# Kernel optimization log

Measured on AMD Instinct MI355X. Metric: run time of the kernel, lower is better.

The kernel has to match this reference:

```python
import jax, jax.numpy as jnp
import numpy as np

NUM_TARGETS = 2
N_ITER = 20
REF_MIC = 1          # 1-based reference mic
CONTRAST = 'laplace'
GAMMA = 1.0
PROJ_BACK = 'mdp'
TOL = 1e-5
EPS_R = 1e-10
REG = 1e-6


def contrast_weights(r, func, gamma, eps_r):
    # phi(r) = g'(r) / r for the chosen contrast function
    r = jnp.maximum(r, eps_r)
    if func == 'laplace':
        return 1.0 / (2.0 * r)
    if func == 'gaussian':
        return jnp.ones_like(r)
    if func == 'power':
        return gamma * r ** (gamma - 2.0)
    raise ValueError(func)


def _iva_forward(X):
    M, T, F, _ = X.shape
    K = NUM_TARGETS
    # (M,T,F,2) real/imag -> complex (F,M,T)
    X_c = jnp.transpose(X[..., 0] + 1j * X[..., 1], (2, 0, 1))
    cdtype = X_c.dtype
    eyeM = jnp.eye(M, dtype=cdtype)
    W_hat = jnp.tile(eyeM[None], (F, 1, 1))
    W_hat = W_hat.at[:, K:, K:].set(-jnp.eye(M - K, dtype=cdtype))
    # input covariance (constant over iterations): (F,M,M)
    C = jnp.einsum('fmt,fnt->fmn', X_c, X_c.conj()) / T
    reg_eye = REG * eyeM  # broadcasts over F / (K,F)
    eps = jnp.finfo(jnp.float32).eps
    done = jnp.array(False)

    for _ in range(N_ITER):
        W_old = W_hat
        # current target estimates: (F,K,T)
        Y = jnp.einsum('fkm,fmt->fkt', W_hat[:, :K, :], X_c)
        r = jnp.sqrt(jnp.maximum((jnp.abs(Y) ** 2).sum(axis=0), EPS_R))  # (K,T)
        w_t = contrast_weights(r, CONTRAST, GAMMA, EPS_R).astype(cdtype)
        # weighted covariances: (K,F,M,M)
        V = jnp.einsum('kt,fmt,fnt->kfmn', w_t, X_c, X_c.conj()) / T
        V_reg = V + reg_eye

        Wn = W_hat
        for k in range(K):
            temp = Wn @ V_reg[k]                              # (F,M,M)
            e_k = jnp.zeros((F, M), dtype=cdtype).at[:, k].set(1.0)
            w_vec = jnp.linalg.solve(temp, e_k[..., None])[..., 0]  # (F,M)
            denom = jnp.sqrt(
                jnp.einsum('fm,fmn,fn->f', w_vec.conj(), V_reg[k], w_vec).real + EPS_R
            )
            Wn = Wn.at[:, k, :].set((w_vec / denom[:, None]).conj())
        # background block: J = solve(tmp[:, :, :K], tmp[:, :, K:])^H
        tmp = Wn[:, :K, :] @ C                                # (F,K,M)
        J = jnp.conj(jnp.swapaxes(jnp.linalg.solve(tmp[:, :, :K], tmp[:, :, K:]), 1, 2))
        Wn = Wn.at[:, K:, :K].set(J)

        rel = jnp.linalg.norm(Wn - W_old) / jnp.maximum(jnp.linalg.norm(W_old), eps)
        W_hat = jnp.where(done, W_old, Wn)  # freeze once converged (mimics break)
        done = done | (rel < TOL)

    W = W_hat[:, :K, :]
    Y = jnp.einsum('fkm,fmt->fkt', W, X_c)  # (F,K,T)
    if REF_MIC is not None and 0 < REF_MIC <= M:
        if PROJ_BACK == 'mdp':
            A = jnp.linalg.pinv(W)               # (F,M,K)
            scale = A[:, REF_MIC - 1, :]         # (F,K)
            Y = scale[:, :, None] * Y
        elif PROJ_BACK == 'scale_constraint':
            Wp = jnp.linalg.pinv(W)
            d = jnp.max(jnp.abs(Wp), axis=1)     # (F,K)
            Y = d[:, :, None].astype(cdtype) * Y
    Y_out = jnp.transpose(Y, (1, 2, 0))          # (K,T,F)
    return jnp.stack([Y_out.real, Y_out.imag], axis=-1)


def setup_inputs() -> dict:
    key = jax.random.key(0)
    X = jax.random.normal(key, (8, 2048, 513, 2), dtype=jnp.float32)
    return {"X": X}


def reference(X):
    return _iva_forward(X)
```

## Files before the change

kernel.cpp:

```cpp
#include <hip/hip_runtime.h>

#define F_ 513
#define M_ 8
#define T_ 2048
#define K_ 2
#define NITER 20
#define REGC 1e-6
#define EPSR 1e-10
#define TOLC 1e-5
#define NG 256
#define TS 4
#define UPB ((F_ + 3) / 4)

typedef double2 cd;
__device__ __forceinline__ cd cmk(double r, double i){ cd z; z.x=r; z.y=i; return z; }
__device__ __forceinline__ cd cadd(cd a, cd b){ return cmk(a.x+b.x, a.y+b.y); }
__device__ __forceinline__ cd csub(cd a, cd b){ return cmk(a.x-b.x, a.y-b.y); }
__device__ __forceinline__ cd cmul(cd a, cd b){ return cmk(a.x*b.x - a.y*b.y, a.x*b.y + a.y*b.x); }
__device__ __forceinline__ cd cconj(cd a){ return cmk(a.x, -a.y); }
__device__ __forceinline__ cd cdiv(cd a, cd b){
  double d = b.x*b.x + b.y*b.y;
  return cmk((a.x*b.x + a.y*b.y)/d, (a.y*b.x - a.x*b.y)/d);
}
__device__ __forceinline__ double cabs2(cd a){ return a.x*a.x + a.y*a.y; }
__device__ __forceinline__ cd shflc(cd v, int l){
  cd r; r.x = __shfl(v.x, l, 64); r.y = __shfl(v.y, l, 64); return r;
}
__device__ __forceinline__ cd sel8(const cd x[8], int idx){
  cd r = x[0];
  #pragma unroll
  for (int q=1;q<8;++q) if (idx==q) r = x[q];
  return r;
}

__device__ __forceinline__ void solve_f(int f, int lane,
    const cd* __restrict__ Vp, const cd* __restrict__ Cp,
    float2* __restrict__ Wg, double* __restrict__ dsum, double* __restrict__ osum)
{
  int i = lane >> 3, j = lane & 7;
  float2 wf = Wg[(size_t)f*64 + lane];
  cd Wn = cmk(wf.x, wf.y);
  cd Wold = Wn;
  cd x[8];
  #pragma unroll
  for (int k=0; k<K_; ++k){
    cd Vr = cmk(0,0);
    #pragma unroll
    for (int s2=0; s2<TS; ++s2)
      Vr = cadd(Vr, Vp[(((size_t)k*F_ + f)*TS + s2)*64 + lane]);
    if (i == j) Vr.x += REGC;
    cd temp = cmk(0,0);
    #pragma unroll
    for (int q=0;q<8;++q) temp = cadd(temp, cmul(shflc(Wn, i*8+q), shflc(Vr, q*8+j)));
    cd b = cmk(i==k ? 1.0 : 0.0, 0.0);
    for (int p=0; p<8; ++p){
      double pv = (j==p && i>=p) ? cabs2(temp) : -1.0;
      int pidx = i;
      for (int off=32; off; off>>=1){
        double ov = __shfl_xor(pv, off, 64);
        int oi = __shfl_xor(pidx, off, 64);
        if (ov > pv){ pv = ov; pidx = oi; }
      }
      cd tp = shflc(temp, pidx*8 + j);
      cd tq = shflc(temp, p*8 + j);
      cd bp_ = shflc(b, pidx*8 + j);
      cd bq_ = shflc(b, p*8 + j);
      if (i == p){ temp = tp; b = bp_; }
      else if (i == pidx){ temp = tq; b = bq_; }
      cd tip = shflc(temp, i*8 + p);
      cd tpp = shflc(temp, p*8 + p);
      cd tpj = shflc(temp, p*8 + j);
      cd bpr = shflc(b, p*8 + j);
      cd fac = cdiv(tip, tpp);
      if (i > p){ temp = csub(temp, cmul(fac, tpj)); b = csub(b, cmul(fac, bpr)); }
    }
    #pragma unroll
    for (int p=7; p>=0; --p){
      cd s = shflc(b, p*8);
      #pragma unroll
      for (int q=p+1; q<8; ++q){
        cd tpq = shflc(temp, p*8 + q);
        s = csub(s, cmul(tpq, x[q]));
      }
      x[p] = cdiv(s, shflc(temp, p*8 + p));
    }
    cd xi = sel8(x, i), xj = sel8(x, j);
    cd z = cmul(cconj(xi), Vr);
    double dl = z.x*xj.x - z.y*xj.y;
    for (int off=32; off; off>>=1) dl += __shfl_xor(dl, off, 64);
    double denom = sqrt(dl + EPSR);
    if (i == k){ Wn = cmk(xj.x/denom, -xj.y/denom); }
  }
  cd Cc = cmk(0,0);
  #pragma unroll
  for (int s2=0; s2<TS; ++s2)
    Cc = cadd(Cc, Cp[((size_t)f*TS + s2)*64 + lane]);
  cd tmp = cmk(0,0);
  #pragma unroll
  for (int q=0;q<8;++q) tmp = cadd(tmp, cmul(shflc(Wn, i*8+q), shflc(Cc, q*8+j)));
  cd A = shflc(tmp, 0), B = shflc(tmp, 1), C2 = shflc(tmp, 8), D = shflc(tmp, 9);
  cd det = csub(cmul(A,D), cmul(B,C2));
  cd t0 = shflc(tmp, i);
  cd t1 = shflc(tmp, 8 + i);
  cd Z0 = cdiv(csub(cmul(D,t0), cmul(B,t1)), det);
  cd Z1 = cdiv(csub(cmul(A,t1), cmul(C2,t0)), det);
  if (i >= K_ && j < K_){
    cd Z = (j==0) ? Z0 : Z1;
    Wn = cconj(Z);
  }
  double ds = cabs2(csub(Wn, Wold));
  double os = cabs2(Wold);
  for (int off=32; off; off>>=1){
    ds += __shfl_xor(ds, off, 64);
    os += __shfl_xor(os, off, 64);
  }
  float2 wo; wo.x = (float)Wn.x; wo.y = (float)Wn.y;
  Wg[(size_t)f*64 + lane] = wo;
  if (lane == 0){ dsum[f] = ds; osum[f] = os; }
}

__global__ __launch_bounds__(256) void pack_kernel(const float2* __restrict__ Xin, float2* __restrict__ Xc){
  __shared__ float tr[32][65];
  __shared__ float ti[32][65];
  int f0 = blockIdx.x*64, t0 = blockIdx.y*32, m = blockIdx.z;
  for (int i = threadIdx.x; i < 32*64; i += 256){
    int tl = i >> 6, fl = i & 63;
    int f = f0 + fl;
    float2 v; v.x = 0.f; v.y = 0.f;
    if (f < F_) v = Xin[((size_t)m*T_ + (t0 + tl))*F_ + f];
    tr[tl][fl] = v.x; ti[tl][fl] = v.y;
  }
  __syncthreads();
  for (int i = threadIdx.x; i < 64*16; i += 256){
    int fl = i >> 4, tl2 = i & 15;
    int f = f0 + fl;
    if (f < F_){
      int t = 2*tl2;
      float4 v;
      v.x = tr[t][fl];   v.y = ti[t][fl];
      v.z = tr[t+1][fl]; v.w = ti[t+1][fl];
      *(float4*)&Xc[((size_t)f*8 + m)*T_ + t0 + t] = v;
    }
  }
}

__global__ __launch_bounds__(512) void cov0_kernel(const float2* __restrict__ Xc, cd* __restrict__ Cp,
                                                   float2* __restrict__ Wg){
  __shared__ float2 xs[8][514];
  __shared__ double wred[2][8][64];
  int f = blockIdx.x, s = blockIdx.y;
  int tid = threadIdx.x;
  int w = tid >> 6, lane = tid & 63;
  int m = lane >> 3, n = lane & 7;
  if (s == 0 && tid < 64){
    int i = tid >> 3, j = tid & 7;
    float v = (i==j) ? (i < K_ ? 1.f : -1.f) : 0.f;
    Wg[(size_t)f*64 + tid] = make_float2(v, 0.f);
  }
  #pragma unroll
  for (int r=0; r<4; ++r){
    int idx = tid + r*512;
    int mm = idx >> 8, q = idx & 255;
    float4 v = ((const float4*)(Xc + ((size_t)f*8 + mm)*T_ + s*512))[q];
    *(float4*)&xs[mm][q*2] = v;
  }
  __syncthreads();
  const float2* xm = xs[m];
  const float2* xn = xs[n];
  int tbase = w*64;
  float ar=0.f, ai=0.f;
  #pragma unroll 8
  for (int tt=0; tt<64; tt+=2){
    float4 av = *(const float4*)&xm[tbase+tt];
    float4 bv = *(const float4*)&xn[tbase+tt];
    ar += fmaf(av.x, bv.x, av.y*bv.y) + fmaf(av.z, bv.z, av.w*bv.w);
    ai += fmaf(av.y, bv.x, -av.x*bv.y) + fmaf(av.w, bv.z, -av.z*bv.w);
  }
  wred[0][w][lane] = ar; wred[1][w][lane] = ai;
  __syncthreads();
  if (tid < 64){
    double sr=0, si=0;
    #pragma unroll
    for (int ww=0; ww<8; ++ww){ sr += wred[0][ww][tid]; si += wred[1][ww][tid]; }
    const double inv = 1.0/(double)T_;
    Cp[((size_t)f*TS + s)*64 + tid] = cmk(sr*inv, si*inv);
  }
}

__global__ __launch_bounds__(256) void yr_kernel(const float2* __restrict__ Xc, const float2* __restrict__ Wg,
                                                 float* __restrict__ part, const int* __restrict__ flags){
  if (*(volatile const int*)flags) return;
  int g = blockIdx.y;
  int t = blockIdx.x*256 + threadIdx.x;
  float acc0 = 0.f, acc1 = 0.f;
  for (int f = g; f < F_; f += NG){
    const float2* Wf = Wg + (size_t)f*64;
    float2 y0; y0.x=0; y0.y=0;
    float2 y1; y1.x=0; y1.y=0;
    #pragma unroll
    for (int m=0;m<8;++m){
      float2 xv = Xc[((size_t)f*8 + m)*T_ + t];
      float2 w0 = Wf[m];
      float2 w1 = Wf[8+m];
      y0.x = fmaf(w0.x,xv.x,fmaf(-w0.y,xv.y,y0.x)); y0.y = fmaf(w0.x,xv.y,fmaf(w0.y,xv.x,y0.y));
      y1.x = fmaf(w1.x,xv.x,fmaf(-w1.y,xv.y,y1.x)); y1.y = fmaf(w1.x,xv.y,fmaf(w1.y,xv.x,y1.y));
    }
    acc0 += y0.x*y0.x + y0.y*y0.y;
    acc1 += y1.x*y1.x + y1.y*y1.y;
  }
  part[((size_t)g*2+0)*T_ + t] = acc0;
  part[((size_t)g*2+1)*T_ + t] = acc1;
}

__global__ __launch_bounds__(256) void rw_kernel(const float* __restrict__ part, float* __restrict__ wts2f,
                                                 const int* __restrict__ flags){
  if (*(volatile const int*)flags) return;
  int v = blockIdx.x*256 + threadIdx.x;
  int k = v >> 11, t = v & (T_-1);
  double s = 0;
  for (int g=0; g<NG; ++g) s += (double)part[((size_t)g*2+k)*T_ + t];
  wts2f[2*t + k] = (float)(0.5 / sqrt(fmax(s, EPSR)));
}

__global__ __launch_bounds__(512, 8) void covF_kernel(const float2* __restrict__ Xc, const float2* __restrict__ wts2,
                                                      cd* __restrict__ Vp, const int* __restrict__ flags){
  if (*(volatile const int*)flags) return;
  __shared__ float2 xs[8][514];
  __shared__ float2 wsm2[512];
  int f = blockIdx.x, s = blockIdx.y;
  int tid = threadIdx.x;
  int w = tid >> 6, lane = tid & 63;
  int m = lane >> 3, n = lane & 7;
  #pragma unroll
  for (int r=0; r<4; ++r){
    int idx = tid + r*512;
    int mm = idx >> 8, q = idx & 255;
    float4 v = ((const float4*)(Xc + ((size_t)f*8 + mm)*T_ + s*512))[q];
    *(float4*)&xs[mm][q*2] = v;
  }
  wsm2[tid] = wts2[s*512 + tid];
  __syncthreads();
  const float2* xm = xs[m];
  const float2* xn = xs[n];
  int tbase = w*64;
  float a0r=0.f, a0i=0.f, a1r=0.f, a1i=0.f;
  #pragma unroll 8
  for (int tt=0; tt<64; tt+=2){
    float4 av = *(const float4*)&xm[tbase+tt];
    float4 bv = *(const float4*)&xn[tbase+tt];
    float zr0 = fmaf(av.x, bv.x, av.y*bv.y);
    float zi0 = fmaf(av.y, bv.x, -av.x*bv.y);
    float zr1 = fmaf(av.z, bv.z, av.w*bv.w);
    float zi1 = fmaf(av.w, bv.z, -av.z*bv.w);
    float4 wv = *(const float4*)&wsm2[tbase+tt];
    a0r = fmaf(wv.x, zr0, a0r); a0i = fmaf(wv.x, zi0, a0i);
    a1r = fmaf(wv.y, zr0, a1r); a1i = fmaf(wv.y, zi0, a1i);
    a0r = fmaf(wv.z, zr1, a0r); a0i = fmaf(wv.z, zi1, a0i);
    a1r = fmaf(wv.w, zr1, a1r); a1i = fmaf(wv.w, zi1, a1i);
  }
  __syncthreads();
  float* wred = (float*)&xs[0][0];
  wred[0*512 + w*64 + lane] = a0r;
  wred[1*512 + w*64 + lane] = a0i;
  wred[2*512 + w*64 + lane] = a1r;
  wred[3*512 + w*64 + lane] = a1i;
  __syncthreads();
  const double inv = 1.0/(double)T_;
  if (tid < 128){
    int k = tid >> 6, l = tid & 63;
    float rr = 0.f, ii = 0.f;
    #pragma unroll
    for (int ww=0; ww<8; ++ww){
      rr += wred[(k*2+0)*512 + ww*64 + l];
      ii += wred[(k*2+1)*512 + ww*64 + l];
    }
    Vp[(((size_t)k*F_ + f)*TS + s)*64 + l] = cmk((double)rr*inv, (double)ii*inv);
  }
}

__global__ __launch_bounds__(256) void updF_kernel(const cd* __restrict__ Vp, const cd* __restrict__ Cp,
                                                   float2* __restrict__ Wg,
                                                   double* __restrict__ dsum, double* __restrict__ osum,
                                                   int* __restrict__ flags){
  if (*(volatile const int*)flags) return;
  int lane = threadIdx.x & 63;
  int w = threadIdx.x >> 6;
  int f = blockIdx.x*4 + w;
  if (f < F_) solve_f(f, lane, Vp, Cp, Wg, dsum, osum);
  __shared__ int lastFlag;
  __threadfence();
  __syncthreads();
  if (threadIdx.x == 0){
    int tk = atomicAdd(&flags[1], 1);
    lastFlag = (tk == UPB-1) ? 1 : 0;
  }
  __syncthreads();
  if (lastFlag && threadIdx.x < 64){
    __threadfence();
    double d=0, o=0;
    for (int idx=lane; idx<F_; idx+=64){
      d += ((volatile double*)dsum)[idx];
      o += ((volatile double*)osum)[idx];
    }
    for (int off=32; off; off>>=1){ d += __shfl_xor(d, off, 64); o += __shfl_xor(o, off, 64); }
    if (lane == 0){
      flags[1] = 0;
      double rel = sqrt(d) / fmax(sqrt(o), 1.1920928955078125e-7);
      if (rel < TOLC) flags[0] = 1;
    }
  }
}

__global__ __launch_bounds__(256) void out_kernel(const float2* __restrict__ Xc, const float2* __restrict__ Wg,
                                                  float2* __restrict__ out){
  __shared__ float re0[32][65], im0[32][65], re1[32][65], im1[32][65];
  __shared__ float2 scl[32][2];
  int f0 = blockIdx.x*32, t0 = blockIdx.y*64;
  int lane = threadIdx.x & 63, w = threadIdx.x >> 6;
  if (threadIdx.x < 32){
    int f = f0 + threadIdx.x;
    if (f < F_){
      cd w0[8], w1[8];
      #pragma unroll
      for (int m=0;m<8;++m){
        float2 a = Wg[(size_t)f*64 + m];     w0[m] = cmk(a.x, a.y);
        float2 b = Wg[(size_t)f*64 + 8 + m]; w1[m] = cmk(b.x, b.y);
      }
      cd G00 = cmk(0,0), G01 = cmk(0,0), G11 = cmk(0,0);
      #pragma unroll
      for (int m=0;m<8;++m){
        G00 = cadd(G00, cmul(w0[m], cconj(w0[m])));
        G01 = cadd(G01, cmul(w0[m], cconj(w1[m])));
        G11 = cadd(G11, cmul(w1[m], cconj(w1[m])));
      }
      cd G10 = cconj(G01);
      cd det = csub(cmul(G00,G11), cmul(G01,G10));
      cd I00 = cdiv(G11, det), I01 = cdiv(cmk(-G01.x,-G01.y), det);
      cd I10 = cdiv(cmk(-G10.x,-G10.y), det), I11 = cdiv(G00, det);
      cd c0 = cconj(w0[0]), c1 = cconj(w1[0]);
      cd s0 = cadd(cmul(c0, I00), cmul(c1, I10));
      cd s1 = cadd(cmul(c0, I01), cmul(c1, I11));
      scl[threadIdx.x][0] = make_float2((float)s0.x, (float)s0.y);
      scl[threadIdx.x][1] = make_float2((float)s1.x, (float)s1.y);
    }
  }
  __syncthreads();
  for (int fl = w; fl < 32; fl += 4){
    int f = f0 + fl;
    if (f < F_){
      const float2* Wf = Wg + (size_t)f*64;
      int t = t0 + lane;
      float2 y0; y0.x=0; y0.y=0;
      float2 y1; y1.x=0; y1.y=0;
      #pragma unroll
      for (int m=0;m<8;++m){
        float2 xv = Xc[((size_t)f*8 + m)*T_ + t];
        float2 w0 = Wf[m];
        float2 w1 = Wf[8+m];
        y0.x += w0.x*xv.x - w0.y*xv.y; y0.y += w0.x*xv.y + w0.y*xv.x;
        y1.x += w1.x*xv.x - w1.y*xv.y; y1.y += w1.x*xv.y + w1.y*xv.x;
      }
      float2 s0 = scl[fl][0];
      float2 s1 = scl[fl][1];
      re0[fl][lane] = s0.x*y0.x - s0.y*y0.y; im0[fl][lane] = s0.x*y0.y + s0.y*y0.x;
      re1[fl][lane] = s1.x*y1.x - s1.y*y1.y; im1[fl][lane] = s1.x*y1.y + s1.y*y1.x;
    }
  }
  __syncthreads();
  for (int i = threadIdx.x; i < 32*64; i += 256){
    int tl = i >> 5, fl = i & 31;
    int f = f0 + fl;
    if (f < F_){
      int t = t0 + tl;
      float2 o0; o0.x = re0[fl][tl]; o0.y = im0[fl][tl];
      float2 o1; o1.x = re1[fl][tl]; o1.y = im1[fl][tl];
      out[((size_t)(0*T_ + t))*F_ + f] = o0;
      out[((size_t)(1*T_ + t))*F_ + f] = o1;
    }
  }
}

extern "C" void kernel_launch(void* const* d_in, const int* in_sizes, int n_in,
                              void* d_out, int out_size, void* d_ws, size_t ws_size,
                              hipStream_t stream) {
  const float2* Xin = (const float2*)d_in[0];
  char* ws = (char*)d_ws;
  size_t off = 0;
  auto alloc = [&](size_t bytes) -> void* {
    void* p = ws + off;
    off += (bytes + 255) & ~(size_t)255;
    return p;
  };
  float2* Xc   = (float2*)alloc((size_t)F_*M_*T_*8);
  cd*     Cp   = (cd*)alloc((size_t)F_*TS*64*16);
  cd*     Vp   = (cd*)alloc((size_t)K_*F_*TS*64*16);
  float2* W    = (float2*)alloc((size_t)F_*64*8);
  float*  part = (float*)alloc((size_t)NG*K_*T_*4);
  float*  wts2 = (float*)alloc((size_t)T_*8);
  double* dsum = (double*)alloc((size_t)F_*8);
  double* osum = (double*)alloc((size_t)F_*8);
  int*    ibuf = (int*)alloc(4096);
  if (off > ws_size) return;
  int* flags = ibuf;

  hipMemsetAsync(ibuf, 0, 4096, stream);

  pack_kernel<<<dim3(9, 64, 8), 256, 0, stream>>>(Xin, Xc);
  cov0_kernel<<<dim3(F_, TS), 512, 0, stream>>>(Xc, Cp, W);

  for (int it=0; it<NITER; ++it){
    yr_kernel<<<dim3(T_/256, NG), 256, 0, stream>>>(Xc, W, part, flags);
    rw_kernel<<<(K_*T_ + 255)/256, 256, 0, stream>>>(part, wts2, flags);
    covF_kernel<<<dim3(F_, TS), 512, 0, stream>>>(Xc, (const float2*)wts2, Vp, flags);
    updF_kernel<<<UPB, 256, 0, stream>>>(Vp, Cp, W, dsum, osum, flags);
  }

  out_kernel<<<dim3(17, 32), 256, 0, stream>>>(Xc, W, (float2*)d_out);
}
```

Baseline: 1.713 ms.

## Run per-frequency solve in fp32 with packed pivot search, split rw reduction

The per-frequency 8x8 complex solve in updF is moved from double to single precision. Its pivot search now packs the magnitude and row index into one unsigned key, so each step needs one shuffle reduction. The rw_kernel spreads the 256-group sum over four warps per block with a shared-memory combine and launches 64 blocks instead of 16. The out_kernel 2x2 Gram inverse is simplified using Hermitian symmetry. The aim is lower latency in the serial update and the weight-reduction kernels, at the cost of reduced numerical accuracy in the solve.

```diff
diff --git a/kernel.cpp b/kernel.cpp
--- a/kernel.cpp
+++ b/kernel.cpp
@@ -5,7 +5,7 @@
 #define T_ 2048
 #define K_ 2
 #define NITER 20
-#define REGC 1e-6
+#define REGC 1e-6f
 #define EPSR 1e-10
 #define TOLC 1e-5
 #define NG 256
@@ -13,109 +13,119 @@
 #define UPB ((F_ + 3) / 4)
 
 typedef double2 cd;
+typedef float2 cf;
 __device__ __forceinline__ cd cmk(double r, double i){ cd z; z.x=r; z.y=i; return z; }
-__device__ __forceinline__ cd cadd(cd a, cd b){ return cmk(a.x+b.x, a.y+b.y); }
-__device__ __forceinline__ cd csub(cd a, cd b){ return cmk(a.x-b.x, a.y-b.y); }
-__device__ __forceinline__ cd cmul(cd a, cd b){ return cmk(a.x*b.x - a.y*b.y, a.x*b.y + a.y*b.x); }
-__device__ __forceinline__ cd cconj(cd a){ return cmk(a.x, -a.y); }
-__device__ __forceinline__ cd cdiv(cd a, cd b){
-  double d = b.x*b.x + b.y*b.y;
-  return cmk((a.x*b.x + a.y*b.y)/d, (a.y*b.x - a.x*b.y)/d);
-}
-__device__ __forceinline__ double cabs2(cd a){ return a.x*a.x + a.y*a.y; }
-__device__ __forceinline__ cd shflc(cd v, int l){
-  cd r; r.x = __shfl(v.x, l, 64); r.y = __shfl(v.y, l, 64); return r;
-}
-__device__ __forceinline__ cd sel8(const cd x[8], int idx){
-  cd r = x[0];
+__device__ __forceinline__ cf cmkf(float r, float i){ cf z; z.x=r; z.y=i; return z; }
+__device__ __forceinline__ cf caddf(cf a, cf b){ return cmkf(a.x+b.x, a.y+b.y); }
+__device__ __forceinline__ cf csubf(cf a, cf b){ return cmkf(a.x-b.x, a.y-b.y); }
+__device__ __forceinline__ cf cmulf(cf a, cf b){ return cmkf(a.x*b.x - a.y*b.y, a.x*b.y + a.y*b.x); }
+__device__ __forceinline__ cf cconjf(cf a){ return cmkf(a.x, -a.y); }
+__device__ __forceinline__ cf cdivf(cf a, cf b){
+  float d = b.x*b.x + b.y*b.y;
+  return cmkf((a.x*b.x + a.y*b.y)/d, (a.y*b.x - a.x*b.y)/d);
+}
+__device__ __forceinline__ float cabs2f(cf a){ return a.x*a.x + a.y*a.y; }
+__device__ __forceinline__ cf shflcf(cf v, int l){
+  cf r; r.x = __shfl(v.x, l, 64); r.y = __shfl(v.y, l, 64); return r;
+}
+__device__ __forceinline__ cf sel8f(const cf x[8], int idx){
+  cf r = x[0];
   #pragma unroll
   for (int q=1;q<8;++q) if (idx==q) r = x[q];
   return r;
 }
 
-__device__ __forceinline__ void solve_f(int f, int lane,
+__device__ __forceinline__ void solve_f32(int f, int lane,
     const cd* __restrict__ Vp, const cd* __restrict__ Cp,
     float2* __restrict__ Wg, double* __restrict__ dsum, double* __restrict__ osum)
 {
   int i = lane >> 3, j = lane & 7;
-  float2 wf = Wg[(size_t)f*64 + lane];
-  cd Wn = cmk(wf.x, wf.y);
-  cd Wold = Wn;
-  cd x[8];
+  cf Wn = Wg[(size_t)f*64 + lane];
+  cf Wold = Wn;
+  cf x[8];
   #pragma unroll
   for (int k=0; k<K_; ++k){
-    cd Vr = cmk(0,0);
-    #pragma unroll
-    for (int s2=0; s2<TS; ++s2)
-      Vr = cadd(Vr, Vp[(((size_t)k*F_ + f)*TS + s2)*64 + lane]);
+    double vr=0, vi=0;
+    #pragma unroll
+    for (int s2=0; s2<TS; ++s2){
+      cd v = Vp[(((size_t)k*F_ + f)*TS + s2)*64 + lane];
+      vr += v.x; vi += v.y;
+    }
+    cf Vr = cmkf((float)vr, (float)vi);
     if (i == j) Vr.x += REGC;
-    cd temp = cmk(0,0);
-    #pragma unroll
-    for (int q=0;q<8;++q) temp = cadd(temp, cmul(shflc(Wn, i*8+q), shflc(Vr, q*8+j)));
-    cd b = cmk(i==k ? 1.0 : 0.0, 0.0);
+    cf temp = cmkf(0.f,0.f);
+    #pragma unroll
+    for (int q=0;q<8;++q) temp = caddf(temp, cmulf(shflcf(Wn, i*8+q), shflcf(Vr, q*8+j)));
+    cf b = cmkf(i==k ? 1.f : 0.f, 0.f);
     for (int p=0; p<8; ++p){
-      double pv = (j==p && i>=p) ? cabs2(temp) : -1.0;
-      int pidx = i;
+      float pv = cabs2f(temp);
+      unsigned pk = (j==p && i>=p) ? ((__float_as_uint(pv) & 0xFFFFFFC0u) | (unsigned)i) : 0u;
+      #pragma unroll
       for (int off=32; off; off>>=1){
-        double ov = __shfl_xor(pv, off, 64);
-        int oi = __shfl_xor(pidx, off, 64);
-        if (ov > pv){ pv = ov; pidx = oi; }
+        unsigned o = __shfl_xor(pk, off, 64);
+        if (o > pk) pk = o;
       }
-      cd tp = shflc(temp, pidx*8 + j);
-      cd tq = shflc(temp, p*8 + j);
-      cd bp_ = shflc(b, pidx*8 + j);
-      cd bq_ = shflc(b, p*8 + j);
+      int pidx = (int)(pk & 63u);
+      cf tp = shflcf(temp, pidx*8 + j);
+      cf tq = shflcf(temp, p*8 + j);
+      cf bp_ = shflcf(b, pidx*8 + j);
+      cf bq_ = shflcf(b, p*8 + j);
       if (i == p){ temp = tp; b = bp_; }
       else if (i == pidx){ temp = tq; b = bq_; }
-      cd tip = shflc(temp, i*8 + p);
-      cd tpp = shflc(temp, p*8 + p);
-      cd tpj = shflc(temp, p*8 + j);
-      cd bpr = shflc(b, p*8 + j);
-      cd fac = cdiv(tip, tpp);
-      if (i > p){ temp = csub(temp, cmul(fac, tpj)); b = csub(b, cmul(fac, bpr)); }
+      cf tip = shflcf(temp, i*8 + p);
+      cf tpp = shflcf(temp, p*8 + p);
+      cf tpj = shflcf(temp, p*8 + j);
+      cf bpr = shflcf(b, p*8 + j);
+      cf fac = cdivf(tip, tpp);
+      if (i > p){ temp = csubf(temp, cmulf(fac, tpj)); b = csubf(b, cmulf(fac, bpr)); }
     }
     #pragma unroll
     for (int p=7; p>=0; --p){
-      cd s = shflc(b, p*8);
+      cf s = shflcf(b, p*8);
       #pragma unroll
       for (int q=p+1; q<8; ++q){
-        cd tpq = shflc(temp, p*8 + q);
-        s = csub(s, cmul(tpq, x[q]));
+        cf tpq = shflcf(temp, p*8 + q);
+        s = csubf(s, cmulf(tpq, x[q]));
       }
-      x[p] = cdiv(s, shflc(temp, p*8 + p));
-    }
-    cd xi = sel8(x, i), xj = sel8(x, j);
-    cd z = cmul(cconj(xi), Vr);
-    double dl = z.x*xj.x - z.y*xj.y;
+      x[p] = cdivf(s, shflcf(temp, p*8 + p));
+    }
+    cf xi = sel8f(x, i), xj = sel8f(x, j);
+    cf z = cmulf(cconjf(xi), Vr);
+    float dl = z.x*xj.x - z.y*xj.y;
+    #pragma unroll
     for (int off=32; off; off>>=1) dl += __shfl_xor(dl, off, 64);
-    double denom = sqrt(dl + EPSR);
-    if (i == k){ Wn = cmk(xj.x/denom, -xj.y/denom); }
-  }
-  cd Cc = cmk(0,0);
-  #pragma unroll
-  for (int s2=0; s2<TS; ++s2)
-    Cc = cadd(Cc, Cp[((size_t)f*TS + s2)*64 + lane]);
-  cd tmp = cmk(0,0);
-  #pragma unroll
-  for (int q=0;q<8;++q) tmp = cadd(tmp, cmul(shflc(Wn, i*8+q), shflc(Cc, q*8+j)));
-  cd A = shflc(tmp, 0), B = shflc(tmp, 1), C2 = shflc(tmp, 8), D = shflc(tmp, 9);
-  cd det = csub(cmul(A,D), cmul(B,C2));
-  cd t0 = shflc(tmp, i);
-  cd t1 = shflc(tmp, 8 + i);
-  cd Z0 = cdiv(csub(cmul(D,t0), cmul(B,t1)), det);
-  cd Z1 = cdiv(csub(cmul(A,t1), cmul(C2,t0)), det);
+    float denom = sqrtf(dl + 1e-10f);
+    if (i == k){ Wn = cmkf(xj.x/denom, -xj.y/denom); }
+  }
+  double cr=0, ci=0;
+  #pragma unroll
+  for (int s2=0; s2<TS; ++s2){
+    cd c = Cp[((size_t)f*TS + s2)*64 + lane];
+    cr += c.x; ci += c.y;
+  }
+  cf Cc = cmkf((float)cr, (float)ci);
+  cf tmp = cmkf(0.f,0.f);
+  #pragma unroll
+  for (int q=0;q<8;++q) tmp = caddf(tmp, cmulf(shflcf(Wn, i*8+q), shflcf(Cc, q*8+j)));
+  cf A = shflcf(tmp, 0), B = shflcf(tmp, 1), C2 = shflcf(tmp, 8), D = shflcf(tmp, 9);
+  cf det = csubf(cmulf(A,D), cmulf(B,C2));
+  cf t0 = shflcf(tmp, i);
+  cf t1 = shflcf(tmp, 8 + i);
+  cf Z0 = cdivf(csubf(cmulf(D,t0), cmulf(B,t1)), det);
+  cf Z1 = cdivf(csubf(cmulf(A,t1), cmulf(C2,t0)), det);
   if (i >= K_ && j < K_){
-    cd Z = (j==0) ? Z0 : Z1;
-    Wn = cconj(Z);
-  }
-  double ds = cabs2(csub(Wn, Wold));
-  double os = cabs2(Wold);
+    cf Z = (j==0) ? Z0 : Z1;
+    Wn = cconjf(Z);
+  }
+  cf dW = csubf(Wn, Wold);
+  double ds = (double)dW.x*dW.x + (double)dW.y*dW.y;
+  double os = (double)Wold.x*Wold.x + (double)Wold.y*Wold.y;
+  #pragma unroll
   for (int off=32; off; off>>=1){
     ds += __shfl_xor(ds, off, 64);
     os += __shfl_xor(os, off, 64);
   }
-  float2 wo; wo.x = (float)Wn.x; wo.y = (float)Wn.y;
-  Wg[(size_t)f*64 + lane] = wo;
+  Wg[(size_t)f*64 + lane] = Wn;
   if (lane == 0){ dsum[f] = ds; osum[f] = os; }
 }
 
@@ -215,11 +225,18 @@
 __global__ __launch_bounds__(256) void rw_kernel(const float* __restrict__ part, float* __restrict__ wts2f,
                                                  const int* __restrict__ flags){
   if (*(volatile const int*)flags) return;
-  int v = blockIdx.x*256 + threadIdx.x;
+  __shared__ double red[4][64];
+  int l = threadIdx.x & 63, s = threadIdx.x >> 6;
+  int v = blockIdx.x*64 + l;
   int k = v >> 11, t = v & (T_-1);
-  double s = 0;
-  for (int g=0; g<NG; ++g) s += (double)part[((size_t)g*2+k)*T_ + t];
-  wts2f[2*t + k] = (float)(0.5 / sqrt(fmax(s, EPSR)));
+  double sum = 0;
+  for (int g=s; g<NG; g+=4) sum += (double)part[((size_t)g*2+k)*T_ + t];
+  red[s][l] = sum;
+  __syncthreads();
+  if (threadIdx.x < 64){
+    double tot = red[0][l] + red[1][l] + red[2][l] + red[3][l];
+    wts2f[2*t + k] = (float)(0.5 / sqrt(fmax(tot, EPSR)));
+  }
 }
 
 __global__ __launch_bounds__(512, 8) void covF_kernel(const float2* __restrict__ Xc, const float2* __restrict__ wts2,
@@ -286,7 +303,7 @@
   int lane = threadIdx.x & 63;
   int w = threadIdx.x >> 6;
   int f = blockIdx.x*4 + w;
-  if (f < F_) solve_f(f, lane, Vp, Cp, Wg, dsum, osum);
+  if (f < F_) solve_f32(f, lane, Vp, Cp, Wg, dsum, osum);
   __shared__ int lastFlag;
   __threadfence();
   __syncthreads();
@@ -329,17 +346,22 @@
       cd G00 = cmk(0,0), G01 = cmk(0,0), G11 = cmk(0,0);
       #pragma unroll
       for (int m=0;m<8;++m){
-        G00 = cadd(G00, cmul(w0[m], cconj(w0[m])));
-        G01 = cadd(G01, cmul(w0[m], cconj(w1[m])));
-        G11 = cadd(G11, cmul(w1[m], cconj(w1[m])));
+        G00.x += w0[m].x*w0[m].x + w0[m].y*w0[m].y;
+        G01.x += w0[m].x*w1[m].x + w0[m].y*w1[m].y;
+        G01.y += w0[m].y*w1[m].x - w0[m].x*w1[m].y;
+        G11.x += w1[m].x*w1[m].x + w1[m].y*w1[m].y;
       }
-      cd G10 = cconj(G01);
-      cd det = csub(cmul(G00,G11), cmul(G01,G10));
-      cd I00 = cdiv(G11, det), I01 = cdiv(cmk(-G01.x,-G01.y), det);
-      cd I10 = cdiv(cmk(-G10.x,-G10.y), det), I11 = cdiv(G00, det);
-      cd c0 = cconj(w0[0]), c1 = cconj(w1[0]);
-      cd s0 = cadd(cmul(c0, I00), cmul(c1, I10));
-      cd s1 = cadd(cmul(c0, I01), cmul(c1, I11));
+      cd det; det.x = G00.x*G11.x - (G01.x*G01.x + G01.y*G01.y); det.y = 0.0;
+      double idet = 1.0 / det.x;
+      cd I00 = cmk(G11.x*idet, 0.0);
+      cd I01 = cmk(-G01.x*idet, -G01.y*idet);
+      cd I10 = cmk(-G01.x*idet,  G01.y*idet);
+      cd I11 = cmk(G00.x*idet, 0.0);
+      cd c0 = cmk(w0[0].x, -w0[0].y), c1 = cmk(w1[0].x, -w1[0].y);
+      cd s0 = cmk(c0.x*I00.x - c0.y*I00.y + c1.x*I10.x - c1.y*I10.y,
+                  c0.x*I00.y + c0.y*I00.x + c1.x*I10.y + c1.y*I10.x);
+      cd s1 = cmk(c0.x*I01.x - c0.y*I01.y + c1.x*I11.x - c1.y*I11.y,
+                  c0.x*I01.y + c0.y*I01.x + c1.x*I11.y + c1.y*I11.x);
       scl[threadIdx.x][0] = make_float2((float)s0.x, (float)s0.y);
       scl[threadIdx.x][1] = make_float2((float)s1.x, (float)s1.y);
     }
@@ -410,7 +432,7 @@
 
   for (int it=0; it<NITER; ++it){
     yr_kernel<<<dim3(T_/256, NG), 256, 0, stream>>>(Xc, W, part, flags);
-    rw_kernel<<<(K_*T_ + 255)/256, 256, 0, stream>>>(part, wts2, flags);
+    rw_kernel<<<64, 256, 0, stream>>>(part, wts2, flags);
     covF_kernel<<<dim3(F_, TS), 512, 0, stream>>>(Xc, (const float2*)wts2, Vp, flags);
     updF_kernel<<<UPB, 256, 0, stream>>>(Vp, Cp, W, dsum, osum, flags);
   }
```

Measured after the change: 1.778 ms. 1.04x slower.
